# Optimization experiments

Measured on AMD Instinct MI355X. Metric: run time of the kernel, lower is better.

The kernel has to match this reference:

```python
import jax, jax.numpy as jnp
import numpy as np

E = 768
H = 8
EXP = 4
HEAD_D = E // H  # 96, also the post-softmax scaling factor


def _layernorm(x, g, b, eps=1e-5):
    mu = jnp.mean(x, axis=-1, keepdims=True)
    var = jnp.var(x, axis=-1, keepdims=True)
    return (x - mu) * jax.lax.rsqrt(var + eps) * g + b


def setup_inputs() -> dict:
    key = jax.random.key(0)
    ks = jax.random.split(key, 12)
    s = 0.02
    inp = {
        "x": jax.random.normal(ks[0], (8, 1024, E), dtype=jnp.float32),
        "ln1_g": jnp.ones((E,), jnp.float32),
        "ln1_b": jnp.zeros((E,), jnp.float32),
        "Wq": jax.random.normal(ks[1], (E, E), jnp.float32) * s,
        "bq": jnp.zeros((E,), jnp.float32),
        "Wk": jax.random.normal(ks[2], (E, E), jnp.float32) * s,
        "bk": jnp.zeros((E,), jnp.float32),
        "Wv": jax.random.normal(ks[3], (E, E), jnp.float32) * s,
        "bv": jnp.zeros((E,), jnp.float32),
        "Wo": jax.random.normal(ks[4], (E, E), jnp.float32) * s,
        "bo": jnp.zeros((E,), jnp.float32),
        "ln2_g": jnp.ones((E,), jnp.float32),
        "ln2_b": jnp.zeros((E,), jnp.float32),
        "W1": jax.random.normal(ks[5], (E, EXP * E), jnp.float32) * s,
        "b1": jnp.zeros((EXP * E,), jnp.float32),
        "W2": jax.random.normal(ks[6], (EXP * E, E), jnp.float32) * s,
        "b2": jnp.zeros((E,), jnp.float32),
    }
    return inp


def reference(x, ln1_g, ln1_b, Wq, bq, Wk, bk, Wv, bv, Wo, bo,
              ln2_g, ln2_b, W1, b1, W2, b2):
    B, N, _ = x.shape
    # --- sub_block_1: LN -> MHA (post-softmax scaling) -> residual ---
    h = _layernorm(x, ln1_g, ln1_b)
    q = (h @ Wq + bq).reshape(B, N, H, HEAD_D).transpose(0, 2, 1, 3)
    k = (h @ Wk + bk).reshape(B, N, H, HEAD_D).transpose(0, 2, 1, 3)
    v = (h @ Wv + bv).reshape(B, N, H, HEAD_D).transpose(0, 2, 1, 3)
    energy = jnp.einsum('bhqd,bhkd->bhqk', q, k)  # NOTE: no pre-softmax scale
    att = jax.nn.softmax(energy, axis=-1) * HEAD_D  # quirky post-softmax scaling
    out = jnp.einsum('bhqk,bhkd->bhqd', att, v)
    out = out.transpose(0, 2, 1, 3).reshape(B, N, E)
    out = out @ Wo + bo
    x = x + out  # residual
    # --- sub_block_2: LN -> GELU-FFN (NO residual, faithful to source) ---
    h = _layernorm(x, ln2_g, ln2_b)
    h = jax.nn.gelu(h @ W1 + b1, approximate=False)
    return h @ W2 + b2
```

## Files before the change

kernel.cpp:

```cpp
#include <hip/hip_runtime.h>
#include <hip/hip_bf16.h>
#include <math.h>

#define DI __device__ __forceinline__

typedef __attribute__((ext_vector_type(8))) __bf16 bf16x8;
typedef __attribute__((ext_vector_type(8))) short short8;
typedef __attribute__((ext_vector_type(4))) float f32x4;
typedef __attribute__((ext_vector_type(4))) int int4v;
typedef __attribute__((ext_vector_type(4))) unsigned short ushort4v;

DI unsigned short f2bf(float f) {
  union { float f; unsigned u; } v; v.f = f;
  unsigned r = v.u + 0x7fffu + ((v.u >> 16) & 1u);
  return (unsigned short)(r >> 16);
}

DI void gload_lds16(const void* g, void* l) {
  __builtin_amdgcn_global_load_lds(
      (const __attribute__((address_space(1))) void*)g,
      (__attribute__((address_space(3))) void*)l, 16, 0, 0);
}

__global__ __launch_bounds__(256) void transpose_cvt(
    const float* __restrict__ in, short* __restrict__ out, int K, int N)
{
  __shared__ float tile[32][33];
  const int tx = threadIdx.x & 31, ty = threadIdx.x >> 5;
  const int n0 = blockIdx.x * 32, k0 = blockIdx.y * 32;
#pragma unroll
  for (int p = 0; p < 4; ++p)
    tile[ty + p * 8][tx] = in[(size_t)(k0 + ty + p * 8) * N + n0 + tx];
  __syncthreads();
#pragma unroll
  for (int p = 0; p < 4; ++p)
    out[(size_t)(n0 + ty + p * 8) * K + k0 + tx] = (short)f2bf(tile[tx][ty + p * 8]);
}

__global__ __launch_bounds__(256) void v_transpose(
    const short* __restrict__ qkv, short* __restrict__ vT)
{
  __shared__ short tile[64][98];
  const int t = threadIdx.x;
  const int bh = blockIdx.x, nt = blockIdx.y;
  const int b = bh >> 3, h = bh & 7;
  const size_t gbase = (size_t)(b * 1024 + nt * 64) * 2304 + 1536 + h * 96;
#pragma unroll
  for (int i = 0; i < 3; ++i) {
    const int p = i * 256 + t;
    const int row = p / 12, cb = p % 12;
    const short8 v = *(const short8*)(qkv + gbase + (size_t)row * 2304 + cb * 8);
#pragma unroll
    for (int j = 0; j < 4; ++j) {
      unsigned pk = (unsigned)(unsigned short)v[2 * j] |
                    ((unsigned)(unsigned short)v[2 * j + 1] << 16);
      *(unsigned*)&tile[row][cb * 8 + 2 * j] = pk;
    }
  }
  __syncthreads();
#pragma unroll
  for (int i = 0; i < 3; ++i) {
    const int p = i * 256 + t;
    const int d = p >> 3, cb = p & 7;
    short8 o;
#pragma unroll
    for (int j = 0; j < 8; ++j) o[j] = tile[cb * 8 + j][d];
    *(short8*)(vT + ((size_t)bh * 96 + d) * 1024 + nt * 64 + cb * 8) = o;
  }
}

__global__ __launch_bounds__(256) void ln_rows(
    const float* __restrict__ x, const float* __restrict__ gw,
    const float* __restrict__ bw, unsigned short* __restrict__ out)
{
  const int wv = threadIdx.x >> 6, ln = threadIdx.x & 63;
  const size_t row = (size_t)blockIdx.x * 4 + wv;
  const float* xr = x + row * 768;
  float4 v[3];
  float s = 0.f, sq = 0.f;
#pragma unroll
  for (int i = 0; i < 3; ++i) {
    v[i] = *(const float4*)(xr + i * 256 + ln * 4);
    s  += v[i].x + v[i].y + v[i].z + v[i].w;
    sq += v[i].x * v[i].x + v[i].y * v[i].y + v[i].z * v[i].z + v[i].w * v[i].w;
  }
#pragma unroll
  for (int msk = 1; msk < 64; msk <<= 1) {
    s  += __shfl_xor(s, msk);
    sq += __shfl_xor(sq, msk);
  }
  const float mean = s * (1.f / 768.f);
  const float var  = sq * (1.f / 768.f) - mean * mean;
  const float rstd = rsqrtf(var + 1e-5f);
#pragma unroll
  for (int i = 0; i < 3; ++i) {
    const int c = i * 256 + ln * 4;
    const float vals[4] = {v[i].x, v[i].y, v[i].z, v[i].w};
    ushort4v o;
#pragma unroll
    for (int j = 0; j < 4; ++j)
      o[j] = f2bf((vals[j] - mean) * rstd * gw[c + j] + bw[c + j]);
    *(ushort4v*)(out + row * 768 + c) = o;
  }
}

enum { EPI_BF16 = 0, EPI_F32_RES = 1, EPI_BF16_GELU = 2, EPI_F32 = 3 };
#define EPITCH 132

template <int MODE, int BM, int BK, int MW>
__global__ __launch_bounds__(256, MW) void gemm_bt(
    const short* __restrict__ A,
    const short* __restrict__ Bt,
    const float* __restrict__ bias,
    const float* __restrict__ resid,
    void* __restrict__ Cout, int ldc,
    int Ntiles, int K)
{
  constexpr int NCHUNK = BK / 8;
  constexpr int CMASK = NCHUNK - 1;
  constexpr int ABYTES = BM * BK * 2;
  constexpr int STAGE_BYTES = (BM + 128) * BK * 2;
  constexpr int NLA = BM * BK / 8 / 256;
  constexpr int NLB = 128 * BK / 8 / 256;
  constexpr int LOADS = NLA + NLB;
  constexpr int MR = BM / 32;
  constexpr int NKK = BK / 32;
  constexpr int SMEM = 2 * STAGE_BYTES > 32 * EPITCH * 4 ? 2 * STAGE_BYTES
                                                         : 32 * EPITCH * 4;
  __shared__ __align__(16) char smem[SMEM];
  const int t = threadIdx.x;
  const int wv = t >> 6, ln = t & 63;
  const int g = ln >> 4, r = ln & 15;
  const int sw = ((int)blockIdx.x & 7) * ((int)gridDim.x >> 3) + ((int)blockIdx.x >> 3);
  const int bm = sw / Ntiles, bn = sw % Ntiles;
  const int wr = wv >> 1, wc = wv & 1;
  f32x4 acc[MR][4] = {};

  auto stage = [&](int buf, int kt) {
    char* as = smem + buf * STAGE_BYTES;
    char* bs = as + ABYTES;
#pragma unroll
    for (int q = 0; q < NLA; ++q) {
      const int p = q * 256 + t;
      const int row = p / NCHUNK, c = (p & CMASK) ^ (row & CMASK);
      gload_lds16(A + (size_t)(bm * BM + row) * K + kt * BK + c * 8,
                  as + q * 4096 + wv * 1024);
    }
#pragma unroll
    for (int q = 0; q < NLB; ++q) {
      const int p = q * 256 + t;
      const int row = p / NCHUNK, c = (p & CMASK) ^ (row & CMASK);
      gload_lds16(Bt + (size_t)(bn * 128 + row) * K + kt * BK + c * 8,
                  bs + q * 4096 + wv * 1024);
    }
  };

  const int nk = K / BK;
  stage(0, 0);
  stage(1, 1);
  int cur = 0;
  for (int kt = 0; kt < nk; ++kt) {
    if (kt + 1 < nk)
      asm volatile("s_waitcnt vmcnt(%0)" :: "n"(LOADS) : "memory");
    else
      asm volatile("s_waitcnt vmcnt(0)" ::: "memory");
    __builtin_amdgcn_s_barrier();
    asm volatile("" ::: "memory");
    const short* as = (const short*)(smem + cur * STAGE_BYTES);
    const short* bs = as + ABYTES / 2;
    bf16x8 af[MR][NKK], bfr[4][NKK];
#pragma unroll
    for (int m = 0; m < MR; ++m) {
      const int row = wr * (BM / 2) + m * 16 + r;
#pragma unroll
      for (int kk = 0; kk < NKK; ++kk)
        af[m][kk] = *(const bf16x8*)(as + row * BK + (((kk * 4 + g) ^ (row & CMASK)) << 3));
    }
#pragma unroll
    for (int n = 0; n < 4; ++n) {
      const int row = wc * 64 + n * 16 + r;
#pragma unroll
      for (int kk = 0; kk < NKK; ++kk)
        bfr[n][kk] = *(const bf16x8*)(bs + row * BK + (((kk * 4 + g) ^ (row & CMASK)) << 3));
    }
    asm volatile("s_waitcnt lgkmcnt(0)" ::: "memory");
    __builtin_amdgcn_sched_barrier(0);
    __builtin_amdgcn_s_barrier();
    if (kt + 2 < nk) stage(cur, kt + 2);
#pragma unroll
    for (int kk = 0; kk < NKK; ++kk)
#pragma unroll
      for (int m = 0; m < MR; ++m)
#pragma unroll
        for (int n = 0; n < 4; ++n)
          acc[m][n] = __builtin_amdgcn_mfma_f32_16x16x32_bf16(af[m][kk], bfr[n][kk],
                                                              acc[m][n], 0, 0, 0);
    cur ^= 1;
  }
  __syncthreads();

  float* epi = (float*)smem;
  const int cq = (t & 7) * 16;
  const int c0 = bn * 128 + cq;
  f32x4 bv[4];
#pragma unroll
  for (int j = 0; j < 4; ++j) bv[j] = *(const f32x4*)(bias + c0 + j * 4);

#pragma unroll
  for (int m = 0; m < MR; ++m) {
#pragma unroll
    for (int n = 0; n < 4; ++n) {
      const int col = wc * 64 + n * 16 + r;
#pragma unroll
      for (int q = 0; q < 4; ++q)
        epi[(wr * 16 + g * 4 + q) * EPITCH + col] = acc[m][n][q];
    }
    __syncthreads();
    const int lr = t >> 3;
    const size_t grow = (size_t)(bm * BM + (lr < 16 ? m * 16 + lr
                                                    : BM / 2 + m * 16 + (lr - 16)));
    float vals[16];
#pragma unroll
    for (int j = 0; j < 4; ++j) {
      const f32x4 vv = *(const f32x4*)(epi + lr * EPITCH + cq + j * 4);
#pragma unroll
      for (int e = 0; e < 4; ++e) vals[j * 4 + e] = vv[e] + bv[j][e];
    }
    if constexpr (MODE == EPI_F32_RES) {
#pragma unroll
      for (int j = 0; j < 4; ++j) {
        const f32x4 rv = *(const f32x4*)(resid + grow * ldc + c0 + j * 4);
#pragma unroll
        for (int e = 0; e < 4; ++e) vals[j * 4 + e] += rv[e];
      }
    }
    if constexpr (MODE == EPI_BF16_GELU) {
#pragma unroll
      for (int j = 0; j < 16; ++j)
        vals[j] = 0.5f * vals[j] * (1.0f + erff(vals[j] * 0.70710678118654752f));
    }
    if constexpr (MODE == EPI_F32 || MODE == EPI_F32_RES) {
      float* op = (float*)Cout + grow * ldc + c0;
#pragma unroll
      for (int j = 0; j < 4; ++j) {
        f32x4 ov;
#pragma unroll
        for (int e = 0; e < 4; ++e) ov[e] = vals[j * 4 + e];
        *(f32x4*)(op + j * 4) = ov;
      }
    } else {
      unsigned short* op = (unsigned short*)Cout + grow * ldc + c0;
#pragma unroll
      for (int hhalf = 0; hhalf < 2; ++hhalf) {
        short8 ov;
#pragma unroll
        for (int e = 0; e < 8; ++e) ov[e] = (short)f2bf(vals[hhalf * 8 + e]);
        *(short8*)(op + hhalf * 8) = ov;
      }
    }
    __syncthreads();
  }
}

__global__ __launch_bounds__(256, 2) void attn_fwd(
    const short* __restrict__ qkv, const short* __restrict__ vT,
    unsigned short* __restrict__ ab)
{
  __shared__ short Ks[2][64 * 128];
  __shared__ short Vs[2][96 * 64];
  __shared__ short Ps[4][16 * 64];
  const int t = threadIdx.x, wv = t >> 6, ln = t & 63;
  const int g = ln >> 4, r = ln & 15;
  const int bid = ((int)blockIdx.x & 7) * 64 + ((int)blockIdx.x >> 3);
  const int bh = bid >> 3, qt = bid & 7;
  const int b = bh >> 3, h = bh & 7;

  bf16x8 qf[2][3];
#pragma unroll
  for (int u = 0; u < 2; ++u) {
    const size_t rowq = (size_t)(b * 1024 + qt * 128 + wv * 32 + u * 16 + r);
#pragma unroll
    for (int kd = 0; kd < 3; ++kd)
      qf[u][kd] = *(const bf16x8*)(qkv + rowq * 2304 + h * 96 + kd * 32 + g * 8);
  }

  size_t offK[4];
#pragma unroll
  for (int i = 0; i < 4; ++i) {
    const int p = i * 256 + t;
    const int row = p >> 4, cb = p & 15, cbs = cb ^ (row & 7);
    offK[i] = (size_t)row * 2304 + 768 + h * 96 + (cbs << 3);
  }
  size_t offV[3];
#pragma unroll
  for (int i = 0; i < 3; ++i) {
    const int p = i * 256 + t;
    const int row = p >> 3, cb = p & 7, cbs = cb ^ (row & 7);
    offV[i] = ((size_t)bh * 96 + row) * 1024 + (cbs << 3);
  }
  const short* qb = qkv + (size_t)b * 1024 * 2304;

  auto stageKV = [&](int buf, int kt) {
    const size_t kadd = (size_t)kt * 64 * 2304;
#pragma unroll
    for (int i = 0; i < 4; ++i)
      gload_lds16(qb + kadd + offK[i], (char*)Ks[buf] + i * 4096 + wv * 1024);
#pragma unroll
    for (int i = 0; i < 3; ++i)
      gload_lds16(vT + offV[i] + kt * 64, (char*)Vs[buf] + i * 4096 + wv * 1024);
  };

  f32x4 o[2][6] = {};
  float mrow[2][4], lrow[2][4];
#pragma unroll
  for (int u = 0; u < 2; ++u)
#pragma unroll
    for (int q = 0; q < 4; ++q) { mrow[u][q] = -1e30f; lrow[u][q] = 0.f; }

  stageKV(0, 0);
  __syncthreads();
  int cur = 0;
  for (int kt = 0; kt < 16; ++kt) {
    if (kt < 15) stageKV(cur ^ 1, kt + 1);
    const short* ks = Ks[cur];
    const short* vs = Vs[cur];

#pragma unroll
    for (int u = 0; u < 2; ++u) {
      f32x4 s[4];
      __builtin_amdgcn_s_setprio(1);
#pragma unroll
      for (int sub = 0; sub < 4; ++sub) {
        f32x4 a = {0.f, 0.f, 0.f, 0.f};
#pragma unroll
        for (int kd = 0; kd < 3; ++kd) {
          const bf16x8 kf = *(const bf16x8*)(
              ks + (sub * 16 + r) * 128 + (((kd * 4 + g) ^ (r & 7)) << 3));
          a = __builtin_amdgcn_mfma_f32_16x16x32_bf16(qf[u][kd], kf, a, 0, 0, 0);
        }
        s[sub] = a;
      }
      __builtin_amdgcn_s_setprio(0);

      float mnew[4], scale[4], tsum[4];
#pragma unroll
      for (int q = 0; q < 4; ++q) {
        float tm = s[0][q];
#pragma unroll
        for (int sub = 1; sub < 4; ++sub) tm = fmaxf(tm, s[sub][q]);
#pragma unroll
        for (int msk = 1; msk < 16; msk <<= 1) tm = fmaxf(tm, __shfl_xor(tm, msk));
        mnew[q] = fmaxf(mrow[u][q], tm);
        scale[q] = __expf(mrow[u][q] - mnew[q]);
        tsum[q] = 0.f;
      }
#pragma unroll
      for (int sub = 0; sub < 4; ++sub) {
#pragma unroll
        for (int q = 0; q < 4; ++q) {
          const float p = __expf(s[sub][q] - mnew[q]);
          tsum[q] += p;
          const int pi = g * 4 + q, pj = sub * 16 + r;
          Ps[wv][pi * 64 + (((pj >> 3) ^ (pi & 7)) << 3) + (pj & 7)] = (short)f2bf(p);
        }
      }
#pragma unroll
      for (int q = 0; q < 4; ++q) {
#pragma unroll
        for (int msk = 1; msk < 16; msk <<= 1) tsum[q] += __shfl_xor(tsum[q], msk);
        lrow[u][q] = lrow[u][q] * scale[q] + tsum[q];
        mrow[u][q] = mnew[q];
      }
#pragma unroll
      for (int nd = 0; nd < 6; ++nd)
#pragma unroll
        for (int q = 0; q < 4; ++q) o[u][nd][q] *= scale[q];

      __builtin_amdgcn_s_setprio(1);
#pragma unroll
      for (int nd = 0; nd < 6; ++nd) {
#pragma unroll
        for (int kk = 0; kk < 2; ++kk) {
          const bf16x8 pf = *(const bf16x8*)(
              Ps[wv] + r * 64 + (((kk * 4 + g) ^ (r & 7)) << 3));
          const bf16x8 vf = *(const bf16x8*)(
              vs + (nd * 16 + r) * 64 + (((kk * 4 + g) ^ (r & 7)) << 3));
          o[u][nd] = __builtin_amdgcn_mfma_f32_16x16x32_bf16(pf, vf, o[u][nd], 0, 0, 0);
        }
      }
      __builtin_amdgcn_s_setprio(0);
    }
    __syncthreads();
    cur ^= 1;
  }

#pragma unroll
  for (int u = 0; u < 2; ++u) {
#pragma unroll
    for (int q = 0; q < 4; ++q) {
      const float inv = 96.0f / lrow[u][q];
      const size_t row = (size_t)(b * 1024 + qt * 128 + wv * 32 + u * 16 + g * 4 + q);
#pragma unroll
      for (int nd = 0; nd < 6; ++nd)
        ab[row * 768 + h * 96 + nd * 16 + r] = f2bf(o[u][nd][q] * inv);
    }
  }
}

extern "C" void kernel_launch(void* const* d_in, const int* in_sizes, int n_in,
                              void* d_out, int out_size, void* d_ws, size_t ws_size,
                              hipStream_t stream)
{
  const float* x    = (const float*)d_in[0];
  const float* ln1g = (const float*)d_in[1];
  const float* ln1b = (const float*)d_in[2];
  const float* Wq   = (const float*)d_in[3];
  const float* bq   = (const float*)d_in[4];
  const float* Wk   = (const float*)d_in[5];
  const float* bk   = (const float*)d_in[6];
  const float* Wv   = (const float*)d_in[7];
  const float* bv   = (const float*)d_in[8];
  const float* Wo   = (const float*)d_in[9];
  const float* bo   = (const float*)d_in[10];
  const float* ln2g = (const float*)d_in[11];
  const float* ln2b = (const float*)d_in[12];
  const float* W1   = (const float*)d_in[13];
  const float* b1   = (const float*)d_in[14];
  const float* W2   = (const float*)d_in[15];
  const float* b2   = (const float*)d_in[16];

  char* ws = (char*)d_ws;
  size_t off = 0;
  short* Wtqkv = (short*)(ws + off); off += (size_t)2304 * 768 * 2;
  short* Wto   = (short*)(ws + off); off += (size_t)768 * 768 * 2;
  short* Wt1   = (short*)(ws + off); off += (size_t)3072 * 768 * 2;
  short* Wt2   = (short*)(ws + off); off += (size_t)768 * 3072 * 2;
  float* bqkv  = (float*)(ws + off); off += 16384;
  short* hb    = (short*)(ws + off); off += (size_t)8192 * 768 * 2;
  short* qkv   = (short*)(ws + off); off += (size_t)8192 * 2304 * 2;
  short* h2b   = (short*)(ws + off); off += (size_t)8192 * 768 * 2;
  short* f1 = hb;
  short* ab = hb;
  short* vT = h2b;
  float* x1 = (float*)d_out;

  transpose_cvt<<<dim3(24, 24), 256, 0, stream>>>(Wq, Wtqkv, 768, 768);
  transpose_cvt<<<dim3(24, 24), 256, 0, stream>>>(Wk, Wtqkv + (size_t)768 * 768, 768, 768);
  transpose_cvt<<<dim3(24, 24), 256, 0, stream>>>(Wv, Wtqkv + (size_t)1536 * 768, 768, 768);
  transpose_cvt<<<dim3(24, 24), 256, 0, stream>>>(Wo, Wto, 768, 768);
  transpose_cvt<<<dim3(96, 24), 256, 0, stream>>>(W1, Wt1, 768, 3072);
  transpose_cvt<<<dim3(24, 96), 256, 0, stream>>>(W2, Wt2, 3072, 768);
  hipMemcpyAsync(bqkv,        bq, 768 * sizeof(float), hipMemcpyDeviceToDevice, stream);
  hipMemcpyAsync(bqkv + 768,  bk, 768 * sizeof(float), hipMemcpyDeviceToDevice, stream);
  hipMemcpyAsync(bqkv + 1536, bv, 768 * sizeof(float), hipMemcpyDeviceToDevice, stream);

  ln_rows<<<2048, 256, 0, stream>>>(x, ln1g, ln1b, (unsigned short*)hb);
  gemm_bt<EPI_BF16, 128, 32, 3><<<64 * 18, 256, 0, stream>>>(hb, Wtqkv, bqkv, nullptr, qkv, 2304, 18, 768);
  v_transpose<<<dim3(64, 16), 256, 0, stream>>>(qkv, vT);
  attn_fwd<<<512, 256, 0, stream>>>(qkv, vT, (unsigned short*)ab);
  gemm_bt<EPI_F32_RES, 64, 64, 3><<<128 * 6, 256, 0, stream>>>(ab, Wto, bo, x, x1, 768, 6, 768);

  ln_rows<<<2048, 256, 0, stream>>>(x1, ln2g, ln2b, (unsigned short*)h2b);
  gemm_bt<EPI_BF16_GELU, 128, 32, 3><<<64 * 24, 256, 0, stream>>>(h2b, Wt1, b1, nullptr, f1, 3072, 24, 768);
  gemm_bt<EPI_F32, 64, 64, 3><<<128 * 6, 256, 0, stream>>>(f1, Wt2, b2, nullptr, (float*)d_out, 768, 6, 3072);
}
```

Before: 286.5 us.

## Restructure attention inner loop with K/V fragment reuse and lazy softmax rescale

The attention loop now loads each K and V fragment once and reuses it for both 16-row query sub-tiles, so the two sub-tiles' QK and PV MFMAs are batched. P gets a per-subtile buffer to allow this. Online-softmax rescaling is skipped unless the new row max exceeds the running max by more than 8, which avoids the exp and accumulator scaling on most tiles. Manual bf16 rounding is replaced with the native __bf16 conversion. The lazy-max threshold lets unnormalized exponentials grow up to e^8, which adds some risk of overflow or lost precision.

```diff
diff --git a/kernel.cpp b/kernel.cpp
--- a/kernel.cpp
+++ b/kernel.cpp
@@ -10,10 +10,11 @@
 typedef __attribute__((ext_vector_type(4))) int int4v;
 typedef __attribute__((ext_vector_type(4))) unsigned short ushort4v;
 
-DI unsigned short f2bf(float f) {
-  union { float f; unsigned u; } v; v.f = f;
-  unsigned r = v.u + 0x7fffu + ((v.u >> 16) & 1u);
-  return (unsigned short)(r >> 16);
+DI short f2bfn(float f) {
+  __bf16 b = (__bf16)f;
+  short s;
+  __builtin_memcpy(&s, &b, 2);
+  return s;
 }
 
 DI void gload_lds16(const void* g, void* l) {
@@ -34,7 +35,7 @@
   __syncthreads();
 #pragma unroll
   for (int p = 0; p < 4; ++p)
-    out[(size_t)(n0 + ty + p * 8) * K + k0 + tx] = (short)f2bf(tile[tx][ty + p * 8]);
+    out[(size_t)(n0 + ty + p * 8) * K + k0 + tx] = f2bfn(tile[tx][ty + p * 8]);
 }
 
 __global__ __launch_bounds__(256) void v_transpose(
@@ -99,7 +100,7 @@
     ushort4v o;
 #pragma unroll
     for (int j = 0; j < 4; ++j)
-      o[j] = f2bf((vals[j] - mean) * rstd * gw[c + j] + bw[c + j]);
+      o[j] = (unsigned short)f2bfn((vals[j] - mean) * rstd * gw[c + j] + bw[c + j]);
     *(ushort4v*)(out + row * 768 + c) = o;
   }
 }
@@ -254,7 +255,7 @@
       for (int hhalf = 0; hhalf < 2; ++hhalf) {
         short8 ov;
 #pragma unroll
-        for (int e = 0; e < 8; ++e) ov[e] = (short)f2bf(vals[hhalf * 8 + e]);
+        for (int e = 0; e < 8; ++e) ov[e] = f2bfn(vals[hhalf * 8 + e]);
         *(short8*)(op + hhalf * 8) = ov;
       }
     }
@@ -268,7 +269,7 @@
 {
   __shared__ short Ks[2][64 * 128];
   __shared__ short Vs[2][96 * 64];
-  __shared__ short Ps[4][16 * 64];
+  __shared__ short Ps[4][2][16 * 64];
   const int t = threadIdx.x, wv = t >> 6, ln = t & 63;
   const int g = ln >> 4, r = ln & 15;
   const int bid = ((int)blockIdx.x & 7) * 64 + ((int)blockIdx.x >> 3);
@@ -325,71 +326,91 @@
     const short* ks = Ks[cur];
     const short* vs = Vs[cur];
 
+    f32x4 s[2][4] = {};
+    __builtin_amdgcn_s_setprio(1);
+#pragma unroll
+    for (int sub = 0; sub < 4; ++sub) {
+      bf16x8 kf[3];
+#pragma unroll
+      for (int kd = 0; kd < 3; ++kd)
+        kf[kd] = *(const bf16x8*)(
+            ks + (sub * 16 + r) * 128 + (((kd * 4 + g) ^ (r & 7)) << 3));
+#pragma unroll
+      for (int u = 0; u < 2; ++u)
+#pragma unroll
+        for (int kd = 0; kd < 3; ++kd)
+          s[u][sub] = __builtin_amdgcn_mfma_f32_16x16x32_bf16(qf[u][kd], kf[kd],
+                                                              s[u][sub], 0, 0, 0);
+    }
+    __builtin_amdgcn_s_setprio(0);
+
 #pragma unroll
     for (int u = 0; u < 2; ++u) {
-      f32x4 s[4];
-      __builtin_amdgcn_s_setprio(1);
+      float tm[4];
+#pragma unroll
+      for (int q = 0; q < 4; ++q) {
+        float m0 = fmaxf(fmaxf(s[u][0][q], s[u][1][q]),
+                         fmaxf(s[u][2][q], s[u][3][q]));
+#pragma unroll
+        for (int msk = 1; msk < 16; msk <<= 1) m0 = fmaxf(m0, __shfl_xor(m0, msk));
+        tm[q] = m0;
+      }
+      const int ok = (tm[0] <= mrow[u][0] + 8.f) & (tm[1] <= mrow[u][1] + 8.f) &
+                     (tm[2] <= mrow[u][2] + 8.f) & (tm[3] <= mrow[u][3] + 8.f);
+      if (!__all(ok)) {
+#pragma unroll
+        for (int q = 0; q < 4; ++q) {
+          const float mnew = fmaxf(mrow[u][q], tm[q]);
+          const float sc = __expf(mrow[u][q] - mnew);
+          lrow[u][q] *= sc;
+          mrow[u][q] = mnew;
+#pragma unroll
+          for (int nd = 0; nd < 6; ++nd) o[u][nd][q] *= sc;
+        }
+      }
+      float tsum[4] = {0.f, 0.f, 0.f, 0.f};
 #pragma unroll
       for (int sub = 0; sub < 4; ++sub) {
-        f32x4 a = {0.f, 0.f, 0.f, 0.f};
-#pragma unroll
-        for (int kd = 0; kd < 3; ++kd) {
-          const bf16x8 kf = *(const bf16x8*)(
-              ks + (sub * 16 + r) * 128 + (((kd * 4 + g) ^ (r & 7)) << 3));
-          a = __builtin_amdgcn_mfma_f32_16x16x32_bf16(qf[u][kd], kf, a, 0, 0, 0);
-        }
-        s[sub] = a;
-      }
-      __builtin_amdgcn_s_setprio(0);
-
-      float mnew[4], scale[4], tsum[4];
-#pragma unroll
-      for (int q = 0; q < 4; ++q) {
-        float tm = s[0][q];
-#pragma unroll
-        for (int sub = 1; sub < 4; ++sub) tm = fmaxf(tm, s[sub][q]);
-#pragma unroll
-        for (int msk = 1; msk < 16; msk <<= 1) tm = fmaxf(tm, __shfl_xor(tm, msk));
-        mnew[q] = fmaxf(mrow[u][q], tm);
-        scale[q] = __expf(mrow[u][q] - mnew[q]);
-        tsum[q] = 0.f;
-      }
-#pragma unroll
-      for (int sub = 0; sub < 4; ++sub) {
 #pragma unroll
         for (int q = 0; q < 4; ++q) {
-          const float p = __expf(s[sub][q] - mnew[q]);
+          const float p = __expf(s[u][sub][q] - mrow[u][q]);
           tsum[q] += p;
           const int pi = g * 4 + q, pj = sub * 16 + r;
-          Ps[wv][pi * 64 + (((pj >> 3) ^ (pi & 7)) << 3) + (pj & 7)] = (short)f2bf(p);
+          Ps[wv][u][pi * 64 + (((pj >> 3) ^ (pi & 7)) << 3) + (pj & 7)] = f2bfn(p);
         }
       }
 #pragma unroll
       for (int q = 0; q < 4; ++q) {
 #pragma unroll
         for (int msk = 1; msk < 16; msk <<= 1) tsum[q] += __shfl_xor(tsum[q], msk);
-        lrow[u][q] = lrow[u][q] * scale[q] + tsum[q];
-        mrow[u][q] = mnew[q];
-      }
-#pragma unroll
-      for (int nd = 0; nd < 6; ++nd)
-#pragma unroll
-        for (int q = 0; q < 4; ++q) o[u][nd][q] *= scale[q];
-
-      __builtin_amdgcn_s_setprio(1);
-#pragma unroll
-      for (int nd = 0; nd < 6; ++nd) {
-#pragma unroll
-        for (int kk = 0; kk < 2; ++kk) {
-          const bf16x8 pf = *(const bf16x8*)(
-              Ps[wv] + r * 64 + (((kk * 4 + g) ^ (r & 7)) << 3));
-          const bf16x8 vf = *(const bf16x8*)(
-              vs + (nd * 16 + r) * 64 + (((kk * 4 + g) ^ (r & 7)) << 3));
-          o[u][nd] = __builtin_amdgcn_mfma_f32_16x16x32_bf16(pf, vf, o[u][nd], 0, 0, 0);
-        }
-      }
-      __builtin_amdgcn_s_setprio(0);
-    }
+        lrow[u][q] += tsum[q];
+      }
+    }
+
+    bf16x8 pf[2][2];
+#pragma unroll
+    for (int u = 0; u < 2; ++u)
+#pragma unroll
+      for (int kk = 0; kk < 2; ++kk)
+        pf[u][kk] = *(const bf16x8*)(
+            Ps[wv][u] + r * 64 + (((kk * 4 + g) ^ (r & 7)) << 3));
+    __builtin_amdgcn_s_setprio(1);
+#pragma unroll
+    for (int nd = 0; nd < 6; ++nd) {
+      bf16x8 vf[2];
+#pragma unroll
+      for (int kk = 0; kk < 2; ++kk)
+        vf[kk] = *(const bf16x8*)(
+            vs + (nd * 16 + r) * 64 + (((kk * 4 + g) ^ (r & 7)) << 3));
+#pragma unroll
+      for (int u = 0; u < 2; ++u)
+#pragma unroll
+        for (int kk = 0; kk < 2; ++kk)
+          o[u][nd] = __builtin_amdgcn_mfma_f32_16x16x32_bf16(pf[u][kk], vf[kk],
+                                                             o[u][nd], 0, 0, 0);
+    }
+    __builtin_amdgcn_s_setprio(0);
+
     __syncthreads();
     cur ^= 1;
   }
@@ -402,7 +423,8 @@
       const size_t row = (size_t)(b * 1024 + qt * 128 + wv * 32 + u * 16 + g * 4 + q);
 #pragma unroll
       for (int nd = 0; nd < 6; ++nd)
-        ab[row * 768 + h * 96 + nd * 16 + r] = f2bf(o[u][nd][q] * inv);
+        ab[row * 768 + h * 96 + nd * 16 + r] =
+            (unsigned short)f2bfn(o[u][nd][q] * inv);
     }
   }
 }
```

Result: faster. 279.6 us (-2.4%).
